# Kernel tuning notes

Hardware: AMD Instinct MI355X
Metric: run time of the kernel (lower is better)

The kernel has to match this reference:

```python
import jax, jax.numpy as jnp
import numpy as np

S, B, D, E = 257, 64, 768, 8
H = 4 * D  # expert hidden dim

def quick_gelu(x):
    return x * jax.nn.sigmoid(1.702 * x)

def setup_inputs() -> dict:
    key = jax.random.key(0)
    ks = jax.random.split(key, 7)
    scale = 1.0 / np.sqrt(D)
    return {
        "x": jax.random.normal(ks[0], (S, B, D), dtype=jnp.float32),
        "W1": jax.random.normal(ks[1], (E, H, D), dtype=jnp.float32) * scale,   # fc1 weight per expert (out,in)
        "b1": jax.random.normal(ks[2], (E, H), dtype=jnp.float32) * 0.01,
        "W2": jax.random.normal(ks[3], (E, D, H), dtype=jnp.float32) * (1.0 / np.sqrt(H)),
        "b2": jax.random.normal(ks[4], (E, D), dtype=jnp.float32) * 0.01,
        "Wr": jax.random.normal(ks[5], (E, D), dtype=jnp.float32) * scale,       # router weight (E, d)
        "br": jnp.zeros((E,), dtype=jnp.float32),
    }

def reference(x, W1, b1, W2, b2, Wr, br):
    s, b, d = x.shape
    xf = x.reshape(s * b, d)                                  # [T, d]
    logits = xf @ Wr.T + br                                   # [T, E]
    probs = jax.nn.softmax(logits, axis=-1)                   # [T, E]
    # all-experts MLP, batched over the expert axis
    h = jnp.einsum('td,ehd->teh', xf, W1) + b1                # [T, E, 4d]
    h = quick_gelu(h)
    outs = jnp.einsum('teh,edh->ted', h, W2) + b2             # [T, E, d]
    y = jnp.einsum('ted,te->td', outs, probs)                 # router-weighted combine
    return y.reshape(s, b, d)
```

## Files before the change

### kernel.cpp

```cpp
#include <hip/hip_runtime.h>

typedef unsigned short u16;
typedef float f32x4 __attribute__((ext_vector_type(4)));
typedef short s16x8 __attribute__((ext_vector_type(8)));

#define T_TOK   16448L
#define D_DIM   768L
#define H_DIM   3072L
#define E_NUM   8L
#define M_PAD   16640L

__device__ __forceinline__ u16 f2bf(float f){
  unsigned u = __float_as_uint(f);
  u = u + 0x7FFFu + ((u >> 16) & 1u);
  return (u16)(u >> 16);
}
__device__ __forceinline__ unsigned f2bf2(float a, float b){
  return (unsigned)f2bf(a) | ((unsigned)f2bf(b) << 16);
}

__device__ __forceinline__ void gload_lds16(const u16* g, u16* s){
  __builtin_amdgcn_global_load_lds((const __attribute__((address_space(1))) void*)g,
                                   (__attribute__((address_space(3))) void*)s,
                                   16, 0, 0);
}

__device__ __forceinline__ int xcd_chunk(int idx, int n){
  const int q = n >> 3, r = n & 7, x = idx & 7;
  return (x < r ? x*(q+1) : r*(q+1) + (x-r)*q) + (idx >> 3);
}

__global__ void k_conv(const float* __restrict__ in, u16* __restrict__ outp,
                       long nValid, long nTotal){
  long i = (long)blockIdx.x * blockDim.x + threadIdx.x;
  long stride = (long)gridDim.x * blockDim.x;
  long n8 = nTotal >> 3;
  for (long v = i; v < n8; v += stride){
    long base = v << 3;
    uint4 o;
    if (base < nValid){
      const float4 f0 = *(const float4*)(in + base);
      const float4 f1 = *(const float4*)(in + base + 4);
      o.x = f2bf2(f0.x, f0.y); o.y = f2bf2(f0.z, f0.w);
      o.z = f2bf2(f1.x, f1.y); o.w = f2bf2(f1.z, f1.w);
    } else {
      o.x = 0u; o.y = 0u; o.z = 0u; o.w = 0u;
    }
    *(uint4*)(outp + base) = o;
  }
}

__global__ void k_router(const float* __restrict__ x, const float* __restrict__ Wr,
                         const float* __restrict__ br, float* __restrict__ probs){
  int w = (int)((blockIdx.x * (long)blockDim.x + threadIdx.x) >> 6);
  int lane = threadIdx.x & 63;
  if (w >= (int)T_TOK) return;
  const float* xr = x + (long)w * D_DIM;
  float l[8];
#pragma unroll
  for (int e = 0; e < 8; ++e) l[e] = 0.f;
#pragma unroll
  for (int c = 0; c < 3; ++c){
    const float4 xv = *(const float4*)(xr + c*256 + lane*4);
#pragma unroll
    for (int e = 0; e < 8; ++e){
      const float4 wv = *(const float4*)(Wr + (long)e*D_DIM + c*256 + lane*4);
      l[e] += xv.x*wv.x + xv.y*wv.y + xv.z*wv.z + xv.w*wv.w;
    }
  }
#pragma unroll
  for (int e = 0; e < 8; ++e){
#pragma unroll
    for (int off = 32; off > 0; off >>= 1) l[e] += __shfl_xor(l[e], off);
    l[e] += br[e];
  }
  float m = l[0];
#pragma unroll
  for (int e = 1; e < 8; ++e) m = fmaxf(m, l[e]);
  float s = 0.f;
#pragma unroll
  for (int e = 0; e < 8; ++e){ l[e] = __expf(l[e] - m); s += l[e]; }
  float inv = 1.f / s;
  if (lane == 0){
    float4 p0 = { l[0]*inv, l[1]*inv, l[2]*inv, l[3]*inv };
    float4 p1 = { l[4]*inv, l[5]*inv, l[6]*inv, l[7]*inv };
    *(float4*)(probs + (long)w*8)     = p0;
    *(float4*)(probs + (long)w*8 + 4) = p1;
  }
}

#define FENCE()  __builtin_amdgcn_sched_barrier(0)
#define BAR()    do{ FENCE(); __builtin_amdgcn_s_barrier(); FENCE(); }while(0)
#define LGK0()   do{ asm volatile("s_waitcnt lgkmcnt(0)" ::: "memory"); FENCE(); }while(0)

__device__ __forceinline__ s16x8 ld_frag(const u16* S, int rbase, int c, int ln){
  const int r = rbase + ln;
  return *(const s16x8*)(S + (r << 6) + ((c ^ (r & 7)) << 3));
}

__device__ __forceinline__ void gemm256(const u16* __restrict__ Ag, long lda,
                                        const u16* __restrict__ Bg, long ldb,
                                        int NT, u16* lds, int tid,
                                        f32x4 (&acc)[8][4]){
  const int l  = tid & 63, w = tid >> 6;
  const int wr = w >> 2,  wc = w & 3;
  const int g4 = l >> 4,  ln = l & 15;

  const int rw = l >> 3;
  const int c8 = (l & 7) ^ rw;
  const u16* gA = Ag + (long)(w*8 + rw) * lda + c8*8;
  const u16* gB = Bg + (long)(w*8 + rw) * ldb + c8*8;
  u16* s0 = lds + w*512;
#define SA(par,T,rnd) gload_lds16(gA + (long)(T)*64 + (long)(rnd)*64*lda, s0 + (par)*32768 + (rnd)*4096)
#define SB(par,T,rnd) gload_lds16(gB + (long)(T)*64 + (long)(rnd)*64*ldb, s0 + (par)*32768 + 16384 + (rnd)*4096)

#pragma unroll
  for (int i = 0; i < 4; ++i) SA(0,0,i);
#pragma unroll
  for (int i = 0; i < 4; ++i) SB(0,0,i);
  SA(1,1,0); SB(1,1,0); SA(1,1,2); SB(1,1,1);
  FENCE();
  asm volatile("s_waitcnt vmcnt(4)" ::: "memory");
  BAR();

  for (int kt = 0; kt < NT; ++kt){
    const int par = kt & 1, oth = par ^ 1;
    const u16* As = lds + par * 32768;
    const u16* Bs = As + 16384;
    const bool st1 = (kt + 1 < NT), st2 = (kt + 2 < NT);
    s16x8 aL[4], aH[4], b0[4], b1[4];

#pragma unroll
    for (int ni = 0; ni < 4; ++ni) b0[ni] = ld_frag(Bs, wc*64 + ni*16, g4, ln);
#pragma unroll
    for (int mi = 0; mi < 4; ++mi) aL[mi] = ld_frag(As, wr*128 + mi*16, g4, ln);
    if (st1){ SA(oth, kt+1, 1); SB(oth, kt+1, 2); }
    BAR(); LGK0();
    __builtin_amdgcn_s_setprio(1);
#pragma unroll
    for (int mi = 0; mi < 4; ++mi)
#pragma unroll
      for (int ni = 0; ni < 4; ++ni)
        acc[mi][ni] = __builtin_amdgcn_mfma_f32_16x16x32_bf16(aL[mi], b0[ni], acc[mi][ni], 0, 0, 0);
    __builtin_amdgcn_s_setprio(0);
    BAR();

#pragma unroll
    for (int ni = 0; ni < 4; ++ni) b1[ni] = ld_frag(Bs, wc*64 + ni*16, 4 + g4, ln);
#pragma unroll
    for (int mi = 0; mi < 4; ++mi) aL[mi] = ld_frag(As, wr*128 + mi*16, 4 + g4, ln);
    if (st1){ SA(oth, kt+1, 3); SB(oth, kt+1, 3); }
    BAR(); LGK0();
    __builtin_amdgcn_s_setprio(1);
#pragma unroll
    for (int mi = 0; mi < 4; ++mi)
#pragma unroll
      for (int ni = 0; ni < 4; ++ni)
        acc[mi][ni] = __builtin_amdgcn_mfma_f32_16x16x32_bf16(aL[mi], b1[ni], acc[mi][ni], 0, 0, 0);
    __builtin_amdgcn_s_setprio(0);
    BAR();

#pragma unroll
    for (int mi = 0; mi < 4; ++mi) aH[mi] = ld_frag(As, wr*128 + 64 + mi*16, g4, ln);
    if (st2){ SA(par, kt+2, 0); SB(par, kt+2, 0); }
    BAR(); LGK0();
    __builtin_amdgcn_s_setprio(1);
#pragma unroll
    for (int mi = 0; mi < 4; ++mi)
#pragma unroll
      for (int ni = 0; ni < 4; ++ni)
        acc[mi+4][ni] = __builtin_amdgcn_mfma_f32_16x16x32_bf16(aH[mi], b0[ni], acc[mi+4][ni], 0, 0, 0);
    __builtin_amdgcn_s_setprio(0);
    BAR();

#pragma unroll
    for (int mi = 0; mi < 4; ++mi) aH[mi] = ld_frag(As, wr*128 + 64 + mi*16, 4 + g4, ln);
    if (st2){ SA(par, kt+2, 2); SB(par, kt+2, 1); }
    BAR(); LGK0();
    __builtin_amdgcn_s_setprio(1);
#pragma unroll
    for (int mi = 0; mi < 4; ++mi)
#pragma unroll
      for (int ni = 0; ni < 4; ++ni)
        acc[mi+4][ni] = __builtin_amdgcn_mfma_f32_16x16x32_bf16(aH[mi], b1[ni], acc[mi+4][ni], 0, 0, 0);
    __builtin_amdgcn_s_setprio(0);

    if (st1){
      FENCE();
      if (st2) asm volatile("s_waitcnt vmcnt(4)" ::: "memory");
      else     asm volatile("s_waitcnt vmcnt(0)" ::: "memory");
      BAR();
    }
  }
#undef SA
#undef SB
}

__global__ __launch_bounds__(512, 2) void k_pair(const u16* __restrict__ xb,
                                                 const u16* __restrict__ w1b,
                                                 const float* __restrict__ b1,
                                                 const u16* __restrict__ w2b,
                                                 const float* __restrict__ b2,
                                                 const float* __restrict__ probs,
                                                 float* __restrict__ out,
                                                 const u16* __restrict__ hbR,
                                                 u16* __restrict__ hbW,
                                                 int e2, int t02,
                                                 int e1, int t01, int mt1, int n2){
  __shared__ alignas(16) u16 lds[65536];
  const int tid = threadIdx.x;
  const int l  = tid & 63, w = tid >> 6;
  const int wr = w >> 2,  wc = w & 3;
  const int g4 = l >> 4,  ln = l & 15;
  const int bx = (int)blockIdx.x;
  f32x4 acc[8][4] = {};

  if (bx < n2){
    const int wg = xcd_chunk(bx, n2);
    const int tx = wg / 3, ty = wg % 3;
    const int m0 = tx << 8, n0 = ty << 8;
    gemm256(hbR + (long)m0 * H_DIM, H_DIM,
            w2b + ((long)e2 * D_DIM + n0) * H_DIM, H_DIM,
            48, lds, tid, acc);
    float bias[4];
#pragma unroll
    for (int ni = 0; ni < 4; ++ni) bias[ni] = b2[(long)e2*D_DIM + n0 + wc*64 + ni*16 + ln];
#pragma unroll
    for (int mi = 0; mi < 8; ++mi){
#pragma unroll
      for (int j = 0; j < 4; ++j){
        const int gt = t02 + m0 + wr*128 + mi*16 + g4*4 + j;
        if (gt < (int)T_TOK){
          const float p = probs[(long)gt*8 + e2];
          float* dst = out + (long)gt * D_DIM + n0 + wc*64;
#pragma unroll
          for (int ni = 0; ni < 4; ++ni){
            const float v = p * (acc[mi][ni][j] + bias[ni]);
            if (e2 == 0) dst[ni*16 + ln] = v;
            else         dst[ni*16 + ln] += v;
          }
        }
      }
    }
  } else {
    const int n1 = (int)gridDim.x - n2;
    const int wg = xcd_chunk(bx - n2, n1);
    const int tx = wg % mt1, ty = wg / mt1;
    const int m0 = tx << 8, n0 = ty << 8;
    gemm256(xb + (long)(t01 + m0) * D_DIM, D_DIM,
            w1b + ((long)e1 * H_DIM + n0) * D_DIM, D_DIM,
            12, lds, tid, acc);
    float bias[4];
#pragma unroll
    for (int ni = 0; ni < 4; ++ni) bias[ni] = b1[(long)e1*H_DIM + n0 + wc*64 + ni*16 + ln];
#pragma unroll
    for (int mi = 0; mi < 8; ++mi){
#pragma unroll
      for (int j = 0; j < 4; ++j){
        const int r = m0 + wr*128 + mi*16 + g4*4 + j;
        u16* dst = hbW + (long)r * H_DIM + n0 + wc*64;
#pragma unroll
        for (int ni = 0; ni < 4; ++ni){
          const float v  = acc[mi][ni][j] + bias[ni];
          const float gl = v / (1.0f + __expf(-1.702f * v));
          dst[ni*16 + ln] = f2bf(gl);
        }
      }
    }
  }
}

extern "C" void kernel_launch(void* const* d_in, const int* in_sizes, int n_in,
                              void* d_out, int out_size, void* d_ws, size_t ws_size,
                              hipStream_t stream){
  const float* x  = (const float*)d_in[0];
  const float* W1 = (const float*)d_in[1];
  const float* b1 = (const float*)d_in[2];
  const float* W2 = (const float*)d_in[3];
  const float* b2 = (const float*)d_in[4];
  const float* Wr = (const float*)d_in[5];
  const float* br = (const float*)d_in[6];
  float* out = (float*)d_out;

  char* ws = (char*)d_ws;
  size_t off = 0;
  auto carve = [&](size_t bytes)->void*{
    void* p = ws + off; off += (bytes + 255) & ~(size_t)255; return p;
  };
  u16*   xb    = (u16*)  carve((size_t)M_PAD * D_DIM * 2);
  u16*   w1b   = (u16*)  carve((size_t)E_NUM * H_DIM * D_DIM * 2);
  u16*   w2b   = (u16*)  carve((size_t)E_NUM * D_DIM * H_DIM * 2);
  float* probs = (float*)carve((size_t)T_TOK * E_NUM * 4);
  u16*   hbA   = (u16*)  carve((size_t)8192 * H_DIM * 2);
  u16*   hbB   = (u16*)  carve((size_t)8448 * H_DIM * 2);

  k_conv<<<dim3(2048), dim3(256), 0, stream>>>(x,  xb,  T_TOK*D_DIM, M_PAD*D_DIM);
  k_conv<<<dim3(2048), dim3(256), 0, stream>>>(W1, w1b, E_NUM*H_DIM*D_DIM, E_NUM*H_DIM*D_DIM);
  k_conv<<<dim3(2048), dim3(256), 0, stream>>>(W2, w2b, E_NUM*D_DIM*H_DIM, E_NUM*D_DIM*H_DIM);
  k_router<<<dim3(4112), dim3(256), 0, stream>>>(x, Wr, br, probs);

  const int MTA = 32, MTB = 33;
  const int T0A = 0,  T0B = 8192;

  auto pair = [&](int e2, const u16* hbR, int t02, int mt2,
                  int e1, u16* hbW, int t01, int mt1){
    const int n2 = mt2 * 3, n1 = mt1 * 12;
    k_pair<<<dim3((unsigned)(n2 + n1)), dim3(512), 0, stream>>>(
        xb, w1b, b1, w2b, b2, probs, out, hbR, hbW,
        e2, t02, e1, t01, mt1, n2);
  };

  pair(0, nullptr, 0, 0, 0, hbA, T0A, MTA);
  for (int e = 0; e < 8; ++e){
    pair(e, hbA, T0A, MTA, e, hbB, T0B, MTB);
    if (e < 7) pair(e, hbB, T0B, MTB, e + 1, hbA, T0A, MTA);
  }
  pair(7, hbB, T0B, MTB, 0, nullptr, 0, 0);
}
```

Baseline: 2.003 ms.

## Fuse prologue kernels into one launch and split-K the final fc2 pass

Merges the three bf16 conversion kernels and the router kernel into a single prologue kernel whose blocks pick their role by block index. This removes three launches and the grid-stride loops. The last fc2-only pair launch now splits K into two halves, doubling its block count so more of the GPU is busy on the tail. Each half adds its partial result into the output with atomicAdd, and only the first half adds the bias. The atomics add contention and make the summation order nondeterministic.

```diff
diff --git a/kernel.cpp b/kernel.cpp
--- a/kernel.cpp
+++ b/kernel.cpp
@@ -30,62 +30,73 @@
   return (x < r ? x*(q+1) : r*(q+1) + (x-r)*q) + (idx >> 3);
 }
 
-__global__ void k_conv(const float* __restrict__ in, u16* __restrict__ outp,
-                       long nValid, long nTotal){
-  long i = (long)blockIdx.x * blockDim.x + threadIdx.x;
-  long stride = (long)gridDim.x * blockDim.x;
-  long n8 = nTotal >> 3;
-  for (long v = i; v < n8; v += stride){
-    long base = v << 3;
+__global__ __launch_bounds__(256) void k_pro(const float* __restrict__ x,
+                                             const float* __restrict__ W1,
+                                             const float* __restrict__ W2,
+                                             const float* __restrict__ Wr,
+                                             const float* __restrict__ br,
+                                             u16* __restrict__ xb,
+                                             u16* __restrict__ w1b,
+                                             u16* __restrict__ w2b,
+                                             float* __restrict__ probs){
+  const int bx = (int)blockIdx.x, tid = threadIdx.x;
+  if (bx < 6240){
+    const long base = ((long)bx*256 + tid) << 3;
     uint4 o;
-    if (base < nValid){
-      const float4 f0 = *(const float4*)(in + base);
-      const float4 f1 = *(const float4*)(in + base + 4);
+    if (base < T_TOK*D_DIM){
+      const float4 f0 = *(const float4*)(x + base);
+      const float4 f1 = *(const float4*)(x + base + 4);
       o.x = f2bf2(f0.x, f0.y); o.y = f2bf2(f0.z, f0.w);
       o.z = f2bf2(f1.x, f1.y); o.w = f2bf2(f1.z, f1.w);
-    } else {
-      o.x = 0u; o.y = 0u; o.z = 0u; o.w = 0u;
-    }
-    *(uint4*)(outp + base) = o;
-  }
-}
-
-__global__ void k_router(const float* __restrict__ x, const float* __restrict__ Wr,
-                         const float* __restrict__ br, float* __restrict__ probs){
-  int w = (int)((blockIdx.x * (long)blockDim.x + threadIdx.x) >> 6);
-  int lane = threadIdx.x & 63;
-  if (w >= (int)T_TOK) return;
-  const float* xr = x + (long)w * D_DIM;
-  float l[8];
-#pragma unroll
-  for (int e = 0; e < 8; ++e) l[e] = 0.f;
-#pragma unroll
-  for (int c = 0; c < 3; ++c){
-    const float4 xv = *(const float4*)(xr + c*256 + lane*4);
+    } else { o.x = o.y = o.z = o.w = 0u; }
+    *(uint4*)(xb + base) = o;
+  } else if (bx < 24672){
+    const int  wsel = (bx < 15456) ? 0 : 1;
+    const long base = ((long)(bx - (wsel ? 15456 : 6240))*256 + tid) << 3;
+    const float* src = wsel ? W2 : W1;
+    u16* dst = wsel ? w2b : w1b;
+    const float4 f0 = *(const float4*)(src + base);
+    const float4 f1 = *(const float4*)(src + base + 4);
+    uint4 o;
+    o.x = f2bf2(f0.x, f0.y); o.y = f2bf2(f0.z, f0.w);
+    o.z = f2bf2(f1.x, f1.y); o.w = f2bf2(f1.z, f1.w);
+    *(uint4*)(dst + base) = o;
+  } else {
+    const int w = (int)(((long)(bx - 24672)*256 + tid) >> 6);
+    const int lane = tid & 63;
+    if (w >= (int)T_TOK) return;
+    const float* xr = x + (long)w * D_DIM;
+    float l[8];
+#pragma unroll
+    for (int e = 0; e < 8; ++e) l[e] = 0.f;
+#pragma unroll
+    for (int c = 0; c < 3; ++c){
+      const float4 xv = *(const float4*)(xr + c*256 + lane*4);
+#pragma unroll
+      for (int e = 0; e < 8; ++e){
+        const float4 wv = *(const float4*)(Wr + (long)e*D_DIM + c*256 + lane*4);
+        l[e] += xv.x*wv.x + xv.y*wv.y + xv.z*wv.z + xv.w*wv.w;
+      }
+    }
 #pragma unroll
     for (int e = 0; e < 8; ++e){
-      const float4 wv = *(const float4*)(Wr + (long)e*D_DIM + c*256 + lane*4);
-      l[e] += xv.x*wv.x + xv.y*wv.y + xv.z*wv.z + xv.w*wv.w;
-    }
-  }
-#pragma unroll
-  for (int e = 0; e < 8; ++e){
-#pragma unroll
-    for (int off = 32; off > 0; off >>= 1) l[e] += __shfl_xor(l[e], off);
-    l[e] += br[e];
-  }
-  float m = l[0];
-#pragma unroll
-  for (int e = 1; e < 8; ++e) m = fmaxf(m, l[e]);
-  float s = 0.f;
-#pragma unroll
-  for (int e = 0; e < 8; ++e){ l[e] = __expf(l[e] - m); s += l[e]; }
-  float inv = 1.f / s;
-  if (lane == 0){
-    float4 p0 = { l[0]*inv, l[1]*inv, l[2]*inv, l[3]*inv };
-    float4 p1 = { l[4]*inv, l[5]*inv, l[6]*inv, l[7]*inv };
-    *(float4*)(probs + (long)w*8)     = p0;
-    *(float4*)(probs + (long)w*8 + 4) = p1;
+#pragma unroll
+      for (int off = 32; off > 0; off >>= 1) l[e] += __shfl_xor(l[e], off);
+      l[e] += br[e];
+    }
+    float m = l[0];
+#pragma unroll
+    for (int e = 1; e < 8; ++e) m = fmaxf(m, l[e]);
+    float s = 0.f;
+#pragma unroll
+    for (int e = 0; e < 8; ++e){ l[e] = __expf(l[e] - m); s += l[e]; }
+    const float inv = 1.f / s;
+    if (lane == 0){
+      float4 p0 = { l[0]*inv, l[1]*inv, l[2]*inv, l[3]*inv };
+      float4 p1 = { l[4]*inv, l[5]*inv, l[6]*inv, l[7]*inv };
+      *(float4*)(probs + (long)w*8)     = p0;
+      *(float4*)(probs + (long)w*8 + 4) = p1;
+    }
   }
 }
 
@@ -206,7 +217,8 @@
                                                  const u16* __restrict__ hbR,
                                                  u16* __restrict__ hbW,
                                                  int e2, int t02,
-                                                 int e1, int t01, int mt1, int n2){
+                                                 int e1, int t01, int mt1, int n2,
+                                                 int spl){
   __shared__ alignas(16) u16 lds[65536];
   const int tid = threadIdx.x;
   const int l  = tid & 63, w = tid >> 6;
@@ -217,14 +229,17 @@
 
   if (bx < n2){
     const int wg = xcd_chunk(bx, n2);
-    const int tx = wg / 3, ty = wg % 3;
+    int tx, ty, sp, nt, koff;
+    if (spl){ ty = wg % 3; sp = (wg / 3) & 1; tx = wg / 6; nt = 24; koff = sp * 1536; }
+    else    { ty = wg % 3; sp = 0;            tx = wg / 3; nt = 48; koff = 0; }
     const int m0 = tx << 8, n0 = ty << 8;
-    gemm256(hbR + (long)m0 * H_DIM, H_DIM,
-            w2b + ((long)e2 * D_DIM + n0) * H_DIM, H_DIM,
-            48, lds, tid, acc);
+    gemm256(hbR + (long)m0 * H_DIM + koff, H_DIM,
+            w2b + ((long)e2 * D_DIM + n0) * H_DIM + koff, H_DIM,
+            nt, lds, tid, acc);
     float bias[4];
 #pragma unroll
-    for (int ni = 0; ni < 4; ++ni) bias[ni] = b2[(long)e2*D_DIM + n0 + wc*64 + ni*16 + ln];
+    for (int ni = 0; ni < 4; ++ni)
+      bias[ni] = (sp == 0) ? b2[(long)e2*D_DIM + n0 + wc*64 + ni*16 + ln] : 0.f;
 #pragma unroll
     for (int mi = 0; mi < 8; ++mi){
 #pragma unroll
@@ -236,8 +251,9 @@
 #pragma unroll
           for (int ni = 0; ni < 4; ++ni){
             const float v = p * (acc[mi][ni][j] + bias[ni]);
-            if (e2 == 0) dst[ni*16 + ln] = v;
-            else         dst[ni*16 + ln] += v;
+            if (spl)          atomicAdd(&dst[ni*16 + ln], v);
+            else if (e2 == 0) dst[ni*16 + ln] = v;
+            else              dst[ni*16 + ln] += v;
           }
         }
       }
@@ -294,26 +310,24 @@
   u16*   hbA   = (u16*)  carve((size_t)8192 * H_DIM * 2);
   u16*   hbB   = (u16*)  carve((size_t)8448 * H_DIM * 2);
 
-  k_conv<<<dim3(2048), dim3(256), 0, stream>>>(x,  xb,  T_TOK*D_DIM, M_PAD*D_DIM);
-  k_conv<<<dim3(2048), dim3(256), 0, stream>>>(W1, w1b, E_NUM*H_DIM*D_DIM, E_NUM*H_DIM*D_DIM);
-  k_conv<<<dim3(2048), dim3(256), 0, stream>>>(W2, w2b, E_NUM*D_DIM*H_DIM, E_NUM*D_DIM*H_DIM);
-  k_router<<<dim3(4112), dim3(256), 0, stream>>>(x, Wr, br, probs);
+  k_pro<<<dim3(28784), dim3(256), 0, stream>>>(x, W1, W2, Wr, br, xb, w1b, w2b, probs);
 
   const int MTA = 32, MTB = 33;
   const int T0A = 0,  T0B = 8192;
 
   auto pair = [&](int e2, const u16* hbR, int t02, int mt2,
-                  int e1, u16* hbW, int t01, int mt1){
-    const int n2 = mt2 * 3, n1 = mt1 * 12;
+                  int e1, u16* hbW, int t01, int mt1, int spl){
+    const int n2 = mt2 * (spl ? 6 : 3);
+    const int n1 = mt1 * 12;
     k_pair<<<dim3((unsigned)(n2 + n1)), dim3(512), 0, stream>>>(
         xb, w1b, b1, w2b, b2, probs, out, hbR, hbW,
-        e2, t02, e1, t01, mt1, n2);
+        e2, t02, e1, t01, mt1, n2, spl);
   };
 
-  pair(0, nullptr, 0, 0, 0, hbA, T0A, MTA);
+  pair(0, nullptr, 0, 0, 0, hbA, T0A, MTA, 0);
   for (int e = 0; e < 8; ++e){
-    pair(e, hbA, T0A, MTA, e, hbB, T0B, MTB);
-    if (e < 7) pair(e, hbB, T0B, MTB, e + 1, hbA, T0A, MTA);
+    pair(e, hbA, T0A, MTA, e, hbB, T0B, MTB, 0);
+    if (e < 7) pair(e, hbB, T0B, MTB, e + 1, hbA, T0A, MTA, 0);
   }
-  pair(7, hbB, T0B, MTB, 0, nullptr, 0, 0);
-}
+  pair(7, hbB, T0B, MTB, 0, nullptr, 0, 0, 1);
+}
```

Measured after the change: 2.013 ms. About the same (+0.5%).
